# Kernel optimization log

Hardware: AMD Instinct MI355X
Metric: run time of the kernel (lower is better)

The kernel has to match this reference:

```python
import jax, jax.numpy as jnp
import numpy as np
from jax import lax

B, N, S, K = 16, 4096, 1024, 32
C_PTS = 64
MLP = [64, 64, 128]
BN_EPS = 1e-5


def _fps(xyz, npoint):
    """Farthest point sampling. xyz: [B,N,3] -> idx [B,npoint] int32."""
    b, n, _ = xyz.shape
    def body(carry, _):
        dist, farthest = carry                       # [B,N], [B]
        centroid = xyz[jnp.arange(b), farthest]      # [B,3]
        d = jnp.sum((xyz - centroid[:, None, :]) ** 2, axis=-1)  # [B,N]
        dist = jnp.minimum(dist, d)
        nxt = jnp.argmax(dist, axis=-1).astype(jnp.int32)
        return (dist, nxt), farthest
    init = (jnp.full((b, n), 1e10, dtype=xyz.dtype), jnp.zeros((b,), jnp.int32))
    _, idxs = lax.scan(body, init, None, length=npoint)  # [npoint, B]
    return idxs.T


def _gather(pts, idx):
    """pts: [B,N,C], idx: [B,S,K] -> [B,S,K,C] (per-batch gather)."""
    return jax.vmap(lambda p, i: p[i])(pts, idx)


def setup_inputs() -> dict:
    key = jax.random.key(0)
    ks = jax.random.split(key, 16)
    inp = {
        "xyz": jax.random.normal(ks[0], (B, N, 3), jnp.float32),
        "points": jax.random.normal(ks[1], (B, N, C_PTS), jnp.float32),
    }
    last = 3 + C_PTS
    ki = 2
    for i, out_c in enumerate(MLP):
        scale = 1.0 / np.sqrt(last)
        inp[f"w{i}"] = jax.random.normal(ks[ki], (last, out_c), jnp.float32) * scale
        inp[f"b{i}"] = jnp.zeros((out_c,), jnp.float32)
        inp[f"g{i}"] = jnp.ones((out_c,), jnp.float32)
        inp[f"be{i}"] = jnp.zeros((out_c,), jnp.float32)
        last = out_c
        ki += 1
    return inp


def _forward(xyz, points, params):
    fps_idx = _fps(xyz, S)                                    # [B,S]
    new_xyz = jnp.take_along_axis(xyz, fps_idx[..., None], axis=1)  # [B,S,3]
    # KNN: pairwise squared distances centroids -> all points
    d = (jnp.sum(new_xyz ** 2, -1)[:, :, None]
         - 2.0 * jnp.einsum('bsc,bnc->bsn', new_xyz, xyz)
         + jnp.sum(xyz ** 2, -1)[:, None, :])                 # [B,S,N]
    _, knn_idx = lax.top_k(-d, K)                             # [B,S,K]
    grouped_xyz = _gather(xyz, knn_idx) - new_xyz[:, :, None, :]   # [B,S,K,3]
    grouped_pts = _gather(points, knn_idx)                    # [B,S,K,C]
    x = jnp.concatenate([grouped_xyz, grouped_pts], axis=-1)  # [B,S,K,3+C]
    for (w, b, g, be) in params:
        x = jnp.einsum('bskc,cd->bskd', x, w) + b             # 1x1 conv
        mean = jnp.mean(x, axis=(0, 1, 2))                    # BN (train stats)
        var = jnp.var(x, axis=(0, 1, 2))
        x = (x - mean) * lax.rsqrt(var + BN_EPS) * g + be
        x = jax.nn.relu(x)
    new_points = jnp.max(x, axis=2)                           # max over nsample
    return new_xyz, new_points


def reference(xyz, points, w0, b0, g0, be0, w1, b1, g1, be1, w2, b2, g2, be2):
    params = [(w0, b0, g0, be0), (w1, b1, g1, be1), (w2, b2, g2, be2)]
    return _forward(xyz, points, params)
```

## Files before the change

### kernel.cpp

```cpp
#include <hip/hip_runtime.h>
#include <float.h>
#include <math.h>

#define B_ 16
#define N_ 4096
#define S_ 1024
#define K_ 32
#define CIN0 67
#define NBS (B_ * S_)
#define NEWXYZ_FLOATS (B_ * S_ * 3)
#define AST 68


__device__ __forceinline__ float sqdist3(float x, float y, float z,
                                         float cx, float cy, float cz) {
#pragma clang fp contract(off)
  float dx = x - cx, dy = y - cy, dz = z - cz;
  float s = dx * dx;
  s = s + dy * dy;
  s = s + dz * dz;
  return s;
}

__device__ __forceinline__ float knn_dist(float c2, float cx, float cy, float cz,
                                          float x, float y, float z) {
#pragma clang fp contract(off)
  float dot = cx * x; dot = dot + cy * y; dot = dot + cz * z;
  float x2 = x * x;   x2 = x2 + y * y;   x2 = x2 + z * z;
  float d = c2 - 2.0f * dot;
  d = d + x2;
  return d;
}

template <int CTRL>
__device__ __forceinline__ float dpp_f(float v, float oldv) {
  return __int_as_float(__builtin_amdgcn_update_dpp(
      __float_as_int(oldv), __float_as_int(v), CTRL, 0xF, 0xF, false));
}
template <int CTRL>
__device__ __forceinline__ int dpp_i(int v, int oldv) {
  return __builtin_amdgcn_update_dpp(oldv, v, CTRL, 0xF, 0xF, false);
}

template <int CTRL>
__device__ __forceinline__ void fps_combine2(float& val, int& idx) {
  const float tv = dpp_f<CTRL>(val, -1.0f);
  const int ti = dpp_i<CTRL>(idx, 0x7fffffff);
  const bool take = (tv > val) || (tv == val && ti < idx);
  val = take ? tv : val;
  idx = take ? ti : idx;
}

__global__ __launch_bounds__(256, 1) void fps_kernel(
    const float* __restrict__ xyz, float* __restrict__ newxyz) {
  const int b = blockIdx.x;
  const int t = threadIdx.x;
  __shared__ float4 sp[N_];
  __shared__ float2 rec[2][4];
  const float* xb = xyz + (size_t)b * N_ * 3;
  for (int p = t; p < N_; p += 256) {
    sp[p] = make_float4(xb[p * 3 + 0], xb[p * 3 + 1], xb[p * 3 + 2], 0.0f);
  }
  float ax[16], ay[16], az[16];
#pragma unroll
  for (int j = 0; j < 16; ++j) {
    const int p = t * 16 + j;
    const float x = xb[p * 3 + 0];
    const float y = xb[p * 3 + 1];
    const float z = xb[p * 3 + 2];
    asm volatile("v_accvgpr_write_b32 %0, %1" : "=a"(ax[j]) : "v"(x));
    asm volatile("v_accvgpr_write_b32 %0, %1" : "=a"(ay[j]) : "v"(y));
    asm volatile("v_accvgpr_write_b32 %0, %1" : "=a"(az[j]) : "v"(z));
  }
  float dist[16];
#pragma unroll
  for (int j = 0; j < 16; ++j) dist[j] = 1e10f;
  __syncthreads();
  float cx = xb[0], cy = xb[1], cz = xb[2];
  for (int s = 0; s < S_; ++s) {
    if (t == 0) {
      float* o = newxyz + ((size_t)b * S_ + s) * 3;
      o[0] = cx; o[1] = cy; o[2] = cz;
    }
    float dd[16];
#pragma unroll
    for (int j = 0; j < 16; ++j) {
      float x, y, z;
      asm volatile("v_accvgpr_read_b32 %0, %1" : "=v"(x) : "a"(ax[j]));
      asm volatile("v_accvgpr_read_b32 %0, %1" : "=v"(y) : "a"(ay[j]));
      asm volatile("v_accvgpr_read_b32 %0, %1" : "=v"(z) : "a"(az[j]));
      dd[j] = sqdist3(x, y, z, cx, cy, cz);
    }
    __builtin_amdgcn_sched_barrier(0);
    float best = -1.0f;
    int bi = 0;
#pragma unroll
    for (int j = 0; j < 16; ++j) {
      const float nd = fminf(dist[j], dd[j]);
      dist[j] = nd;
      const bool take = nd > best;
      best = take ? nd : best;
      bi = take ? (t * 16 + j) : bi;
    }
    fps_combine2<0x111>(best, bi);
    fps_combine2<0x112>(best, bi);
    fps_combine2<0x114>(best, bi);
    fps_combine2<0x118>(best, bi);
    fps_combine2<0x142>(best, bi);
    fps_combine2<0x143>(best, bi);
    const float wv = __int_as_float(__builtin_amdgcn_readlane(__float_as_int(best), 63));
    const int wi = __builtin_amdgcn_readlane(bi, 63);
    const int par = s & 1;
    if ((t & 63) == 0) {
      rec[par][t >> 6] = make_float2(wv, __int_as_float(wi));
    }
    __syncthreads();
    float2 r0 = rec[par][0];
    float bv = r0.x;
    int bj = __float_as_int(r0.y);
#pragma unroll
    for (int w = 1; w < 4; ++w) {
      const float2 r = rec[par][w];
      const int iw = __float_as_int(r.y);
      const bool take = (r.x > bv) || (r.x == bv && iw < bj);
      bv = take ? r.x : bv;
      bj = take ? iw : bj;
    }
    const float4 c = sp[bj];
    cx = c.x; cy = c.y; cz = c.z;
  }
}

__global__ __launch_bounds__(256, 2) void knn_kernel(
    const float* __restrict__ xyz, const float* __restrict__ newxyz,
    int* __restrict__ knn_idx) {
  const int bs0 = blockIdx.x * 4;
  const int b = bs0 >> 10;
  const int t = threadIdx.x;
  const int wave = t >> 6;
  const int lane = t & 63;
  __shared__ float sxx[N_];
  __shared__ float sxy[N_];
  __shared__ float sxz[N_];
  const float* xb = xyz + (size_t)b * N_ * 3;
  for (int p = t; p < N_; p += 256) {
    sxx[p] = xb[p * 3 + 0];
    sxy[p] = xb[p * 3 + 1];
    sxz[p] = xb[p * 3 + 2];
  }
  __syncthreads();
  const int bs = bs0 + wave;
  const float cx = newxyz[(size_t)bs * 3 + 0];
  const float cy = newxyz[(size_t)bs * 3 + 1];
  const float cz = newxyz[(size_t)bs * 3 + 2];
  float c2;
  {
#pragma clang fp contract(off)
    float s = cx * cx;
    s = s + cy * cy;
    s = s + cz * cz;
    c2 = s;
  }
  float d[64];
  float gval[8];
  int gidx[8];
#pragma unroll
  for (int g = 0; g < 8; ++g) {
    float gv = FLT_MAX;
    int gi = g * 8;
#pragma unroll
    for (int q = 0; q < 8; ++q) {
      const int j = g * 8 + q;
      const int p = j * 64 + lane;
      const float dd = knn_dist(c2, cx, cy, cz, sxx[p], sxy[p], sxz[p]);
      d[j] = dd;
      if (dd < gv) { gv = dd; gi = j; }
    }
    gval[g] = gv; gidx[g] = gi;
  }
  int* krow = knn_idx + (size_t)bs * K_;
  for (int it = 0; it < K_; ++it) {
    float best = gval[0];
    int bj = gidx[0];
#pragma unroll
    for (int g = 1; g < 8; ++g) {
      if (gval[g] < best || (gval[g] == best && gidx[g] < bj)) { best = gval[g]; bj = gidx[g]; }
    }
    int bidx = bj * 64 + lane;
#pragma unroll
    for (int off = 32; off >= 1; off >>= 1) {
      const float ov = __shfl_xor(best, off);
      const int oi = __shfl_xor(bidx, off);
      if (ov < best || (ov == best && oi < bidx)) { best = ov; bidx = oi; }
    }
    if (lane == 0) krow[it] = bidx;
    if (lane == (bidx & 63)) {
      const int jl = bidx >> 6;
      const int gg = jl >> 3;
      const int qq = jl & 7;
#pragma unroll
      for (int g = 0; g < 8; ++g) {
        if (g == gg) {
#pragma unroll
          for (int q = 0; q < 8; ++q) {
            d[g * 8 + q] = (q == qq) ? FLT_MAX : d[g * 8 + q];
          }
          float gv = FLT_MAX;
          int gi = g * 8;
#pragma unroll
          for (int q = 0; q < 8; ++q) {
            const int j = g * 8 + q;
            if (d[j] < gv) { gv = d[j]; gi = j; }
          }
          gval[g] = gv; gidx[g] = gi;
        }
      }
    }
  }
}


__device__ __forceinline__ void loadw(float* __restrict__ wbuf,
                                      const float* __restrict__ w, int n, int t) {
  for (int i = t; i < n; i += 256) wbuf[i] = w[i];
}

__device__ __forceinline__ void loadw_half(float* __restrict__ wbuf,
                                           const float* __restrict__ w2, int ofs, int t) {
  for (int i = t; i < 64 * 64; i += 256) {
    const int c = i >> 6, j = i & 63;
    wbuf[i] = w2[c * 128 + ofs + j];
  }
}

__device__ __forceinline__ void build_x0(float* __restrict__ act,
    const float* __restrict__ xyz, const float* __restrict__ points,
    const int* __restrict__ knn_idx, const float* __restrict__ newxyz,
    int bs, int t) {
  const int b = bs >> 10;
  const int* krow = knn_idx + (size_t)bs * K_;
  const float cx = newxyz[(size_t)bs * 3 + 0];
  const float cy = newxyz[(size_t)bs * 3 + 1];
  const float cz = newxyz[(size_t)bs * 3 + 2];
  for (int i = t; i < K_ * CIN0; i += 256) {
    const int k = i / CIN0;
    const int c = i - k * CIN0;
    const int p = krow[k];
    float v;
    if (c < 3) {
      v = xyz[((size_t)b * N_ + p) * 3 + c] - (c == 0 ? cx : (c == 1 ? cy : cz));
    } else {
      v = points[((size_t)b * N_ + p) * 64 + (c - 3)];
    }
    act[k * AST + c] = v;
  }
}

template <int CIN>
__device__ __forceinline__ void matmul64(const float* __restrict__ act,
    const float* __restrict__ wbuf, const float* __restrict__ bias,
    float* __restrict__ out, int t) {
  const int k = t >> 3;
  const int g = t & 7;
  float acc[8];
#pragma unroll
  for (int j = 0; j < 8; ++j) acc[j] = bias[g * 8 + j];
  for (int c = 0; c < CIN; ++c) {
    const float xv = act[k * AST + c];
#pragma unroll
    for (int j = 0; j < 8; ++j) acc[j] += xv * wbuf[c * 64 + g * 8 + j];
  }
#pragma unroll
  for (int j = 0; j < 8; ++j) out[k * AST + g * 8 + j] = acc[j];
}

__device__ __forceinline__ void norm_relu64(float* __restrict__ act,
    const float* __restrict__ scale, const float* __restrict__ shift, int t) {
  for (int i = t; i < K_ * 64; i += 256) {
    const int k = i >> 6, c = i & 63;
    const float v = act[k * AST + c] * scale[c] + shift[c];
    act[k * AST + c] = fmaxf(v, 0.0f);
  }
}

__device__ __forceinline__ void stats64(const float* __restrict__ out,
    float* __restrict__ psum, float* __restrict__ psq, int bs, int ofs, int t) {
  if (t < 64) {
    float s = 0.f, q = 0.f;
    for (int k = 0; k < K_; ++k) {
      const float v = out[k * AST + t];
      s += v; q += v * v;
    }
    psum[(size_t)bs * 128 + ofs + t] = s;
    psq[(size_t)bs * 128 + ofs + t] = q;
  }
}

__device__ __forceinline__ void minmax64(const float* __restrict__ out,
    float* __restrict__ maxraw, float* __restrict__ minbuf, int bs, int ofs, int t) {
  if (t >= 64 && t < 128) {
    const int ch = t - 64;
    float mx = -FLT_MAX, mn = FLT_MAX;
    for (int k = 0; k < K_; ++k) {
      const float v = out[k * AST + ch];
      mx = fmaxf(mx, v); mn = fminf(mn, v);
    }
    maxraw[(size_t)bs * 128 + ofs + ch] = mx;
    minbuf[(size_t)bs * 128 + ofs + ch] = mn;
  }
}


__global__ __launch_bounds__(256) void passA_store_kernel(
    const float* __restrict__ xyz, const float* __restrict__ points,
    const float* __restrict__ newxyz, const int* __restrict__ knn_idx,
    const float* __restrict__ w0, const float* __restrict__ b0,
    float* __restrict__ psum, float* __restrict__ psq, float* __restrict__ zbuf) {
  __shared__ float actA[K_ * AST];
  __shared__ float outB[K_ * AST];
  __shared__ float wbuf[CIN0 * 64];
  const int bs = blockIdx.x, t = threadIdx.x;
  build_x0(actA, xyz, points, knn_idx, newxyz, bs, t);
  loadw(wbuf, w0, CIN0 * 64, t);
  __syncthreads();
  matmul64<CIN0>(actA, wbuf, b0, outB, t);
  __syncthreads();
  stats64(outB, psum, psq, bs, 0, t);
  float* zrow = zbuf + (size_t)bs * 2048;
  for (int i = t; i < 2048; i += 256) zrow[i] = outB[(i >> 6) * AST + (i & 63)];
}

__global__ __launch_bounds__(256) void passB_z_kernel(
    const float* __restrict__ w1, const float* __restrict__ b1,
    const float* __restrict__ scales, const float* __restrict__ shifts,
    float* __restrict__ psum, float* __restrict__ psq, float* __restrict__ zbuf) {
  __shared__ float actA[K_ * AST];
  __shared__ float outB[K_ * AST];
  __shared__ float wbuf[64 * 64];
  const int bs = blockIdx.x, t = threadIdx.x;
  float* zrow = zbuf + (size_t)bs * 2048;
  for (int i = t; i < 2048; i += 256) outB[(i >> 6) * AST + (i & 63)] = zrow[i];
  loadw(wbuf, w1, 64 * 64, t);
  __syncthreads();
  norm_relu64(outB, scales, shifts, t);
  __syncthreads();
  matmul64<64>(outB, wbuf, b1, actA, t);
  __syncthreads();
  stats64(actA, psum, psq, bs, 0, t);
  for (int i = t; i < 2048; i += 256) zrow[i] = actA[(i >> 6) * AST + (i & 63)];
}

__global__ __launch_bounds__(256) void passC_z_kernel(
    const float* __restrict__ w2, const float* __restrict__ b2,
    const float* __restrict__ scales1, const float* __restrict__ shifts1,
    float* __restrict__ psum, float* __restrict__ psq,
    float* __restrict__ maxraw, float* __restrict__ minbuf,
    const float* __restrict__ zbuf) {
  __shared__ float actA[K_ * AST];
  __shared__ float outB[K_ * AST];
  __shared__ float wbuf[64 * 64];
  const int bs = blockIdx.x, t = threadIdx.x;
  const float* zrow = zbuf + (size_t)bs * 2048;
  for (int i = t; i < 2048; i += 256) actA[(i >> 6) * AST + (i & 63)] = zrow[i];
  loadw_half(wbuf, w2, 0, t);
  __syncthreads();
  norm_relu64(actA, scales1, shifts1, t);
  __syncthreads();
  matmul64<64>(actA, wbuf, b2, outB, t);
  __syncthreads();
  stats64(outB, psum, psq, bs, 0, t);
  minmax64(outB, maxraw, minbuf, bs, 0, t);
  loadw_half(wbuf, w2, 64, t);
  __syncthreads();
  matmul64<64>(actA, wbuf, b2 + 64, outB, t);
  __syncthreads();
  stats64(outB, psum, psq, bs, 64, t);
  minmax64(outB, maxraw, minbuf, bs, 64, t);
}


__global__ __launch_bounds__(256) void passA_kernel(
    const float* __restrict__ xyz, const float* __restrict__ points,
    const float* __restrict__ newxyz, const int* __restrict__ knn_idx,
    const float* __restrict__ w0, const float* __restrict__ b0,
    float* __restrict__ psum, float* __restrict__ psq) {
  __shared__ float actA[K_ * AST];
  __shared__ float outB[K_ * AST];
  __shared__ float wbuf[CIN0 * 64];
  const int bs = blockIdx.x, t = threadIdx.x;
  build_x0(actA, xyz, points, knn_idx, newxyz, bs, t);
  loadw(wbuf, w0, CIN0 * 64, t);
  __syncthreads();
  matmul64<CIN0>(actA, wbuf, b0, outB, t);
  __syncthreads();
  stats64(outB, psum, psq, bs, 0, t);
}

__global__ __launch_bounds__(256) void passB_kernel(
    const float* __restrict__ xyz, const float* __restrict__ points,
    const float* __restrict__ newxyz, const int* __restrict__ knn_idx,
    const float* __restrict__ w0, const float* __restrict__ b0,
    const float* __restrict__ w1, const float* __restrict__ b1,
    const float* __restrict__ scales, const float* __restrict__ shifts,
    float* __restrict__ psum, float* __restrict__ psq) {
  __shared__ float actA[K_ * AST];
  __shared__ float outB[K_ * AST];
  __shared__ float wbuf[CIN0 * 64];
  const int bs = blockIdx.x, t = threadIdx.x;
  build_x0(actA, xyz, points, knn_idx, newxyz, bs, t);
  loadw(wbuf, w0, CIN0 * 64, t);
  __syncthreads();
  matmul64<CIN0>(actA, wbuf, b0, outB, t);
  __syncthreads();
  norm_relu64(outB, scales, shifts, t);
  loadw(wbuf, w1, 64 * 64, t);
  __syncthreads();
  matmul64<64>(outB, wbuf, b1, actA, t);
  __syncthreads();
  stats64(actA, psum, psq, bs, 0, t);
}

__global__ __launch_bounds__(256) void passC_kernel(
    const float* __restrict__ xyz, const float* __restrict__ points,
    const float* __restrict__ newxyz, const int* __restrict__ knn_idx,
    const float* __restrict__ w0, const float* __restrict__ b0,
    const float* __restrict__ w1, const float* __restrict__ b1,
    const float* __restrict__ w2, const float* __restrict__ b2,
    const float* __restrict__ scales, const float* __restrict__ shifts,
    float* __restrict__ psum, float* __restrict__ psq,
    float* __restrict__ maxraw, float* __restrict__ minbuf) {
  __shared__ float actA[K_ * AST];
  __shared__ float outB[K_ * AST];
  __shared__ float wbuf[CIN0 * 64];
  const int bs = blockIdx.x, t = threadIdx.x;
  build_x0(actA, xyz, points, knn_idx, newxyz, bs, t);
  loadw(wbuf, w0, CIN0 * 64, t);
  __syncthreads();
  matmul64<CIN0>(actA, wbuf, b0, outB, t);
  __syncthreads();
  norm_relu64(outB, scales, shifts, t);
  loadw(wbuf, w1, 64 * 64, t);
  __syncthreads();
  matmul64<64>(outB, wbuf, b1, actA, t);
  __syncthreads();
  norm_relu64(actA, scales + 128, shifts + 128, t);
  loadw_half(wbuf, w2, 0, t);
  __syncthreads();
  matmul64<64>(actA, wbuf, b2, outB, t);
  __syncthreads();
  stats64(outB, psum, psq, bs, 0, t);
  minmax64(outB, maxraw, minbuf, bs, 0, t);
  loadw_half(wbuf, w2, 64, t);
  __syncthreads();
  matmul64<64>(actA, wbuf, b2 + 64, outB, t);
  __syncthreads();
  stats64(outB, psum, psq, bs, 64, t);
  minmax64(outB, maxraw, minbuf, bs, 64, t);
}

__global__ __launch_bounds__(256) void finalize_kernel(
    const float* __restrict__ psum, const float* __restrict__ psq,
    const float* __restrict__ g, const float* __restrict__ be,
    float* __restrict__ scale, float* __restrict__ shift) {
  const int ch = blockIdx.x, t = threadIdx.x;
  __shared__ float ss[256];
  __shared__ float sq[256];
  float s = 0.f, q = 0.f;
  for (int p = t; p < NBS; p += 256) {
    s += psum[(size_t)p * 128 + ch];
    q += psq[(size_t)p * 128 + ch];
  }
  ss[t] = s; sq[t] = q;
  __syncthreads();
  for (int off = 128; off >= 1; off >>= 1) {
    if (t < off) { ss[t] += ss[t + off]; sq[t] += sq[t + off]; }
    __syncthreads();
  }
  if (t == 0) {
    const float invN = 1.0f / (float)(B_ * S_ * K_);
    const float mean = ss[0] * invN;
    const float var = sq[0] * invN - mean * mean;
    const float sc = g[ch] / sqrtf(var + 1e-5f);
    scale[ch] = sc;
    shift[ch] = be[ch] - mean * sc;
  }
}

__global__ __launch_bounds__(256) void final_kernel(
    const float* __restrict__ minbuf, const float* __restrict__ scale,
    const float* __restrict__ shift, float* __restrict__ out) {
  const int i = blockIdx.x * 256 + threadIdx.x;
  const int ch = i & 127;
  const float sc = scale[ch], sh = shift[ch];
  const float mx = out[NEWXYZ_FLOATS + i];
  const float mn = minbuf[i];
  const float v = sc * (sc >= 0.f ? mx : mn) + sh;
  out[NEWXYZ_FLOATS + i] = fmaxf(v, 0.f);
}

extern "C" void kernel_launch(void* const* d_in, const int* in_sizes, int n_in,
                              void* d_out, int out_size, void* d_ws, size_t ws_size,
                              hipStream_t stream) {
  const float* xyz = (const float*)d_in[0];
  const float* points = (const float*)d_in[1];
  const float* w0 = (const float*)d_in[2];
  const float* b0 = (const float*)d_in[3];
  const float* g0 = (const float*)d_in[4];
  const float* be0 = (const float*)d_in[5];
  const float* w1 = (const float*)d_in[6];
  const float* b1 = (const float*)d_in[7];
  const float* g1 = (const float*)d_in[8];
  const float* be1 = (const float*)d_in[9];
  const float* w2 = (const float*)d_in[10];
  const float* b2 = (const float*)d_in[11];
  const float* g2 = (const float*)d_in[12];
  const float* be2 = (const float*)d_in[13];
  float* out = (float*)d_out;
  float* newxyz = out;
  float* maxraw = out + NEWXYZ_FLOATS;

  float* ws = (float*)d_ws;
  const size_t NEED_FAST =
      (size_t)(524288 + 16384 * 2048 + 2 * NBS * 128 + 768 + NBS * 128) * 4;

  fps_kernel<<<B_, 256, 0, stream>>>(xyz, newxyz);

  if (ws_size >= NEED_FAST) {
    int* knn_idx = (int*)ws;
    float* zbuf = ws + 524288;
    float* psum = zbuf + (size_t)16384 * 2048;
    float* psq = psum + (size_t)NBS * 128;
    float* scales = psq + (size_t)NBS * 128;
    float* shifts = scales + 384;
    float* minbuf = shifts + 384;
    knn_kernel<<<NBS / 4, 256, 0, stream>>>(xyz, newxyz, knn_idx);
    passA_store_kernel<<<NBS, 256, 0, stream>>>(xyz, points, newxyz, knn_idx, w0, b0,
                                                psum, psq, zbuf);
    finalize_kernel<<<64, 256, 0, stream>>>(psum, psq, g0, be0, scales, shifts);
    passB_z_kernel<<<NBS, 256, 0, stream>>>(w1, b1, scales, shifts, psum, psq, zbuf);
    finalize_kernel<<<64, 256, 0, stream>>>(psum, psq, g1, be1, scales + 128, shifts + 128);
    passC_z_kernel<<<NBS, 256, 0, stream>>>(w2, b2, scales + 128, shifts + 128,
                                            psum, psq, maxraw, minbuf, zbuf);
    finalize_kernel<<<128, 256, 0, stream>>>(psum, psq, g2, be2, scales + 256, shifts + 256);
    final_kernel<<<(B_ * S_ * 128) / 256, 256, 0, stream>>>(minbuf, scales + 256,
                                                            shifts + 256, out);
  } else {
    int* knn_idx = (int*)ws;
    float* psum = ws + 524288;
    float* psq = psum + (size_t)NBS * 128;
    float* scales = psq + (size_t)NBS * 128;
    float* shifts = scales + 384;
    float* minbuf = shifts + 384;
    knn_kernel<<<NBS / 4, 256, 0, stream>>>(xyz, newxyz, knn_idx);
    passA_kernel<<<NBS, 256, 0, stream>>>(xyz, points, newxyz, knn_idx, w0, b0, psum, psq);
    finalize_kernel<<<64, 256, 0, stream>>>(psum, psq, g0, be0, scales, shifts);
    passB_kernel<<<NBS, 256, 0, stream>>>(xyz, points, newxyz, knn_idx, w0, b0, w1, b1,
                                          scales, shifts, psum, psq);
    finalize_kernel<<<64, 256, 0, stream>>>(psum, psq, g1, be1, scales + 128, shifts + 128);
    passC_kernel<<<NBS, 256, 0, stream>>>(xyz, points, newxyz, knn_idx, w0, b0, w1, b1, w2, b2,
                                          scales, shifts, psum, psq, maxraw, minbuf);
    finalize_kernel<<<128, 256, 0, stream>>>(psum, psq, g2, be2, scales + 256, shifts + 256);
    final_kernel<<<(B_ * S_ * 128) / 256, 256, 0, stream>>>(minbuf, scales + 256,
                                                            shifts + 256, out);
  }
}
```

Measured before the change: 2.035 ms.

## Fuse FPS and KNN into persistent kernel with per-batch progress flags

Merges the serial FPS kernel and the KNN kernel into one persistent kernel. The first 16 blocks run FPS at raised priority and publish per-batch progress counters with release stores. The other blocks pull KNN tasks from an atomic queue and spin until the centroids they need exist, so KNN overlaps the long FPS phase instead of waiting for it to finish. The matmul inner loop also switches to float4 shared-memory loads with aligned buffers. The risks are spin-wait overhead, contention between the co-resident KNN blocks and the FPS blocks, and a dependence on all FPS blocks being resident, which could deadlock otherwise.

```diff
diff --git a/kernel.cpp b/kernel.cpp
--- a/kernel.cpp
+++ b/kernel.cpp
@@ -10,6 +10,7 @@
 #define NBS (B_ * S_)
 #define NEWXYZ_FLOATS (B_ * S_ * 3)
 #define AST 68
+#define TASKS 4096
 
 
 __device__ __forceinline__ float sqdist3(float x, float y, float z,
@@ -51,171 +52,194 @@
   idx = take ? ti : idx;
 }
 
-__global__ __launch_bounds__(256, 1) void fps_kernel(
-    const float* __restrict__ xyz, float* __restrict__ newxyz) {
-  const int b = blockIdx.x;
+__global__ __launch_bounds__(256, 2) void fused_fps_knn_kernel(
+    const float* __restrict__ xyz, float* __restrict__ newxyz,
+    int* __restrict__ knn_idx, int* __restrict__ ctrl) {
+  __shared__ float sx[N_];
+  __shared__ float sy[N_];
+  __shared__ float sz[N_];
+  __shared__ float2 rec[2][4];
+  __shared__ int sh_tq;
   const int t = threadIdx.x;
-  __shared__ float4 sp[N_];
-  __shared__ float2 rec[2][4];
-  const float* xb = xyz + (size_t)b * N_ * 3;
-  for (int p = t; p < N_; p += 256) {
-    sp[p] = make_float4(xb[p * 3 + 0], xb[p * 3 + 1], xb[p * 3 + 2], 0.0f);
-  }
-  float ax[16], ay[16], az[16];
-#pragma unroll
-  for (int j = 0; j < 16; ++j) {
-    const int p = t * 16 + j;
-    const float x = xb[p * 3 + 0];
-    const float y = xb[p * 3 + 1];
-    const float z = xb[p * 3 + 2];
-    asm volatile("v_accvgpr_write_b32 %0, %1" : "=a"(ax[j]) : "v"(x));
-    asm volatile("v_accvgpr_write_b32 %0, %1" : "=a"(ay[j]) : "v"(y));
-    asm volatile("v_accvgpr_write_b32 %0, %1" : "=a"(az[j]) : "v"(z));
-  }
-  float dist[16];
-#pragma unroll
-  for (int j = 0; j < 16; ++j) dist[j] = 1e10f;
-  __syncthreads();
-  float cx = xb[0], cy = xb[1], cz = xb[2];
-  for (int s = 0; s < S_; ++s) {
+
+  if (blockIdx.x < B_) {
+    __builtin_amdgcn_s_setprio(3);
+    const int b = blockIdx.x;
+    const float* xb = xyz + (size_t)b * N_ * 3;
+    for (int p = t; p < N_; p += 256) {
+      sx[p] = xb[p * 3 + 0];
+      sy[p] = xb[p * 3 + 1];
+      sz[p] = xb[p * 3 + 2];
+    }
+    float ax[16], ay[16], az[16];
+#pragma unroll
+    for (int j = 0; j < 16; ++j) {
+      const int p = t * 16 + j;
+      const float x = xb[p * 3 + 0];
+      const float y = xb[p * 3 + 1];
+      const float z = xb[p * 3 + 2];
+      asm volatile("v_accvgpr_write_b32 %0, %1" : "=a"(ax[j]) : "v"(x));
+      asm volatile("v_accvgpr_write_b32 %0, %1" : "=a"(ay[j]) : "v"(y));
+      asm volatile("v_accvgpr_write_b32 %0, %1" : "=a"(az[j]) : "v"(z));
+    }
+    float dist[16];
+#pragma unroll
+    for (int j = 0; j < 16; ++j) dist[j] = 1e10f;
+    __syncthreads();
+    float cx = xb[0], cy = xb[1], cz = xb[2];
+    for (int s = 0; s < S_; ++s) {
+      if (t == 0) {
+        float* o = newxyz + ((size_t)b * S_ + s) * 3;
+        o[0] = cx; o[1] = cy; o[2] = cz;
+        __hip_atomic_store(&ctrl[1 + b], s + 1, __ATOMIC_RELEASE,
+                           __HIP_MEMORY_SCOPE_AGENT);
+      }
+      float dd[16];
+#pragma unroll
+      for (int j = 0; j < 16; ++j) {
+        float x, y, z;
+        asm volatile("v_accvgpr_read_b32 %0, %1" : "=v"(x) : "a"(ax[j]));
+        asm volatile("v_accvgpr_read_b32 %0, %1" : "=v"(y) : "a"(ay[j]));
+        asm volatile("v_accvgpr_read_b32 %0, %1" : "=v"(z) : "a"(az[j]));
+        dd[j] = sqdist3(x, y, z, cx, cy, cz);
+      }
+      __builtin_amdgcn_sched_barrier(0);
+      float best = -1.0f;
+      int bi = 0;
+#pragma unroll
+      for (int j = 0; j < 16; ++j) {
+        const float nd = fminf(dist[j], dd[j]);
+        dist[j] = nd;
+        const bool take = nd > best;
+        best = take ? nd : best;
+        bi = take ? (t * 16 + j) : bi;
+      }
+      fps_combine2<0x111>(best, bi);
+      fps_combine2<0x112>(best, bi);
+      fps_combine2<0x114>(best, bi);
+      fps_combine2<0x118>(best, bi);
+      fps_combine2<0x142>(best, bi);
+      fps_combine2<0x143>(best, bi);
+      const float wv = __int_as_float(__builtin_amdgcn_readlane(__float_as_int(best), 63));
+      const int wi = __builtin_amdgcn_readlane(bi, 63);
+      const int par = s & 1;
+      if ((t & 63) == 0) {
+        rec[par][t >> 6] = make_float2(wv, __int_as_float(wi));
+      }
+      __syncthreads();
+      float2 r0 = rec[par][0];
+      float bv = r0.x;
+      int bj = __float_as_int(r0.y);
+#pragma unroll
+      for (int w = 1; w < 4; ++w) {
+        const float2 r = rec[par][w];
+        const int iw = __float_as_int(r.y);
+        const bool take = (r.x > bv) || (r.x == bv && iw < bj);
+        bv = take ? r.x : bv;
+        bj = take ? iw : bj;
+      }
+      cx = sx[bj]; cy = sy[bj]; cz = sz[bj];
+    }
+    __builtin_amdgcn_s_setprio(0);
+    __syncthreads();
+  }
+
+  while (true) {
+    if (t == 0) sh_tq = atomicAdd(&ctrl[0], 1);
+    __syncthreads();
+    const int tq = sh_tq;
+    if (tq >= TASKS) break;
+    const int b = tq & 15;
+    const int sg = tq >> 4;
     if (t == 0) {
-      float* o = newxyz + ((size_t)b * S_ + s) * 3;
-      o[0] = cx; o[1] = cy; o[2] = cz;
-    }
-    float dd[16];
-#pragma unroll
-    for (int j = 0; j < 16; ++j) {
-      float x, y, z;
-      asm volatile("v_accvgpr_read_b32 %0, %1" : "=v"(x) : "a"(ax[j]));
-      asm volatile("v_accvgpr_read_b32 %0, %1" : "=v"(y) : "a"(ay[j]));
-      asm volatile("v_accvgpr_read_b32 %0, %1" : "=v"(z) : "a"(az[j]));
-      dd[j] = sqdist3(x, y, z, cx, cy, cz);
-    }
-    __builtin_amdgcn_sched_barrier(0);
-    float best = -1.0f;
-    int bi = 0;
-#pragma unroll
-    for (int j = 0; j < 16; ++j) {
-      const float nd = fminf(dist[j], dd[j]);
-      dist[j] = nd;
-      const bool take = nd > best;
-      best = take ? nd : best;
-      bi = take ? (t * 16 + j) : bi;
-    }
-    fps_combine2<0x111>(best, bi);
-    fps_combine2<0x112>(best, bi);
-    fps_combine2<0x114>(best, bi);
-    fps_combine2<0x118>(best, bi);
-    fps_combine2<0x142>(best, bi);
-    fps_combine2<0x143>(best, bi);
-    const float wv = __int_as_float(__builtin_amdgcn_readlane(__float_as_int(best), 63));
-    const int wi = __builtin_amdgcn_readlane(bi, 63);
-    const int par = s & 1;
-    if ((t & 63) == 0) {
-      rec[par][t >> 6] = make_float2(wv, __int_as_float(wi));
-    }
-    __syncthreads();
-    float2 r0 = rec[par][0];
-    float bv = r0.x;
-    int bj = __float_as_int(r0.y);
-#pragma unroll
-    for (int w = 1; w < 4; ++w) {
-      const float2 r = rec[par][w];
-      const int iw = __float_as_int(r.y);
-      const bool take = (r.x > bv) || (r.x == bv && iw < bj);
-      bv = take ? r.x : bv;
-      bj = take ? iw : bj;
-    }
-    const float4 c = sp[bj];
-    cx = c.x; cy = c.y; cz = c.z;
-  }
-}
-
-__global__ __launch_bounds__(256, 2) void knn_kernel(
-    const float* __restrict__ xyz, const float* __restrict__ newxyz,
-    int* __restrict__ knn_idx) {
-  const int bs0 = blockIdx.x * 4;
-  const int b = bs0 >> 10;
-  const int t = threadIdx.x;
-  const int wave = t >> 6;
-  const int lane = t & 63;
-  __shared__ float sxx[N_];
-  __shared__ float sxy[N_];
-  __shared__ float sxz[N_];
-  const float* xb = xyz + (size_t)b * N_ * 3;
-  for (int p = t; p < N_; p += 256) {
-    sxx[p] = xb[p * 3 + 0];
-    sxy[p] = xb[p * 3 + 1];
-    sxz[p] = xb[p * 3 + 2];
-  }
-  __syncthreads();
-  const int bs = bs0 + wave;
-  const float cx = newxyz[(size_t)bs * 3 + 0];
-  const float cy = newxyz[(size_t)bs * 3 + 1];
-  const float cz = newxyz[(size_t)bs * 3 + 2];
-  float c2;
-  {
+      while (__hip_atomic_load(&ctrl[1 + b], __ATOMIC_ACQUIRE,
+                               __HIP_MEMORY_SCOPE_AGENT) < sg * 4 + 4) {
+        __builtin_amdgcn_s_sleep(2);
+      }
+    }
+    __syncthreads();
+    const float* xb = xyz + (size_t)b * N_ * 3;
+    for (int p = t; p < N_; p += 256) {
+      sx[p] = xb[p * 3 + 0];
+      sy[p] = xb[p * 3 + 1];
+      sz[p] = xb[p * 3 + 2];
+    }
+    __syncthreads();
+    {
+      const int wave = t >> 6;
+      const int lane = t & 63;
+      const int bs = b * S_ + sg * 4 + wave;
+      const float cx = newxyz[(size_t)bs * 3 + 0];
+      const float cy = newxyz[(size_t)bs * 3 + 1];
+      const float cz = newxyz[(size_t)bs * 3 + 2];
+      float c2;
+      {
 #pragma clang fp contract(off)
-    float s = cx * cx;
-    s = s + cy * cy;
-    s = s + cz * cz;
-    c2 = s;
-  }
-  float d[64];
-  float gval[8];
-  int gidx[8];
-#pragma unroll
-  for (int g = 0; g < 8; ++g) {
-    float gv = FLT_MAX;
-    int gi = g * 8;
-#pragma unroll
-    for (int q = 0; q < 8; ++q) {
-      const int j = g * 8 + q;
-      const int p = j * 64 + lane;
-      const float dd = knn_dist(c2, cx, cy, cz, sxx[p], sxy[p], sxz[p]);
-      d[j] = dd;
-      if (dd < gv) { gv = dd; gi = j; }
-    }
-    gval[g] = gv; gidx[g] = gi;
-  }
-  int* krow = knn_idx + (size_t)bs * K_;
-  for (int it = 0; it < K_; ++it) {
-    float best = gval[0];
-    int bj = gidx[0];
-#pragma unroll
-    for (int g = 1; g < 8; ++g) {
-      if (gval[g] < best || (gval[g] == best && gidx[g] < bj)) { best = gval[g]; bj = gidx[g]; }
-    }
-    int bidx = bj * 64 + lane;
-#pragma unroll
-    for (int off = 32; off >= 1; off >>= 1) {
-      const float ov = __shfl_xor(best, off);
-      const int oi = __shfl_xor(bidx, off);
-      if (ov < best || (ov == best && oi < bidx)) { best = ov; bidx = oi; }
-    }
-    if (lane == 0) krow[it] = bidx;
-    if (lane == (bidx & 63)) {
-      const int jl = bidx >> 6;
-      const int gg = jl >> 3;
-      const int qq = jl & 7;
+        float s = cx * cx;
+        s = s + cy * cy;
+        s = s + cz * cz;
+        c2 = s;
+      }
+      float d[64];
+      float gval[8];
+      int gidx[8];
 #pragma unroll
       for (int g = 0; g < 8; ++g) {
-        if (g == gg) {
-#pragma unroll
-          for (int q = 0; q < 8; ++q) {
-            d[g * 8 + q] = (q == qq) ? FLT_MAX : d[g * 8 + q];
+        float gv = FLT_MAX;
+        int gi = g * 8;
+#pragma unroll
+        for (int q = 0; q < 8; ++q) {
+          const int j = g * 8 + q;
+          const int p = j * 64 + lane;
+          const float dd = knn_dist(c2, cx, cy, cz, sx[p], sy[p], sz[p]);
+          d[j] = dd;
+          if (dd < gv) { gv = dd; gi = j; }
+        }
+        gval[g] = gv; gidx[g] = gi;
+      }
+      int* krow = knn_idx + (size_t)bs * K_;
+      for (int it = 0; it < K_; ++it) {
+        float best = gval[0];
+        int bj = gidx[0];
+#pragma unroll
+        for (int g = 1; g < 8; ++g) {
+          if (gval[g] < best || (gval[g] == best && gidx[g] < bj)) {
+            best = gval[g]; bj = gidx[g];
           }
-          float gv = FLT_MAX;
-          int gi = g * 8;
-#pragma unroll
-          for (int q = 0; q < 8; ++q) {
-            const int j = g * 8 + q;
-            if (d[j] < gv) { gv = d[j]; gi = j; }
+        }
+        int bidx = bj * 64 + lane;
+#pragma unroll
+        for (int off = 32; off >= 1; off >>= 1) {
+          const float ov = __shfl_xor(best, off);
+          const int oi = __shfl_xor(bidx, off);
+          if (ov < best || (ov == best && oi < bidx)) { best = ov; bidx = oi; }
+        }
+        if (lane == 0) krow[it] = bidx;
+        if (lane == (bidx & 63)) {
+          const int jl = bidx >> 6;
+          const int gg = jl >> 3;
+          const int qr = jl & 7;
+#pragma unroll
+          for (int g = 0; g < 8; ++g) {
+            if (g == gg) {
+#pragma unroll
+              for (int q = 0; q < 8; ++q) {
+                d[g * 8 + q] = (q == qr) ? FLT_MAX : d[g * 8 + q];
+              }
+              float gv = FLT_MAX;
+              int gi = g * 8;
+#pragma unroll
+              for (int q = 0; q < 8; ++q) {
+                const int j = g * 8 + q;
+                if (d[j] < gv) { gv = d[j]; gi = j; }
+              }
+              gval[g] = gv; gidx[g] = gi;
+            }
           }
-          gval[g] = gv; gidx[g] = gi;
         }
       }
     }
+    __syncthreads();
   }
 }
 
@@ -267,11 +291,15 @@
   for (int j = 0; j < 8; ++j) acc[j] = bias[g * 8 + j];
   for (int c = 0; c < CIN; ++c) {
     const float xv = act[k * AST + c];
-#pragma unroll
-    for (int j = 0; j < 8; ++j) acc[j] += xv * wbuf[c * 64 + g * 8 + j];
-  }
-#pragma unroll
-  for (int j = 0; j < 8; ++j) out[k * AST + g * 8 + j] = acc[j];
+    const float4 wa = *(const float4*)&wbuf[c * 64 + g * 8];
+    const float4 wb = *(const float4*)&wbuf[c * 64 + g * 8 + 4];
+    acc[0] += xv * wa.x; acc[1] += xv * wa.y;
+    acc[2] += xv * wa.z; acc[3] += xv * wa.w;
+    acc[4] += xv * wb.x; acc[5] += xv * wb.y;
+    acc[6] += xv * wb.z; acc[7] += xv * wb.w;
+  }
+  *(float4*)&out[k * AST + g * 8] = make_float4(acc[0], acc[1], acc[2], acc[3]);
+  *(float4*)&out[k * AST + g * 8 + 4] = make_float4(acc[4], acc[5], acc[6], acc[7]);
 }
 
 __device__ __forceinline__ void norm_relu64(float* __restrict__ act,
@@ -316,9 +344,9 @@
     const float* __restrict__ newxyz, const int* __restrict__ knn_idx,
     const float* __restrict__ w0, const float* __restrict__ b0,
     float* __restrict__ psum, float* __restrict__ psq, float* __restrict__ zbuf) {
-  __shared__ float actA[K_ * AST];
-  __shared__ float outB[K_ * AST];
-  __shared__ float wbuf[CIN0 * 64];
+  __shared__ __align__(16) float actA[K_ * AST];
+  __shared__ __align__(16) float outB[K_ * AST];
+  __shared__ __align__(16) float wbuf[CIN0 * 64];
   const int bs = blockIdx.x, t = threadIdx.x;
   build_x0(actA, xyz, points, knn_idx, newxyz, bs, t);
   loadw(wbuf, w0, CIN0 * 64, t);
@@ -334,9 +362,9 @@
     const float* __restrict__ w1, const float* __restrict__ b1,
     const float* __restrict__ scales, const float* __restrict__ shifts,
     float* __restrict__ psum, float* __restrict__ psq, float* __restrict__ zbuf) {
-  __shared__ float actA[K_ * AST];
-  __shared__ float outB[K_ * AST];
-  __shared__ float wbuf[64 * 64];
+  __shared__ __align__(16) float actA[K_ * AST];
+  __shared__ __align__(16) float outB[K_ * AST];
+  __shared__ __align__(16) float wbuf[64 * 64];
   const int bs = blockIdx.x, t = threadIdx.x;
   float* zrow = zbuf + (size_t)bs * 2048;
   for (int i = t; i < 2048; i += 256) outB[(i >> 6) * AST + (i & 63)] = zrow[i];
@@ -356,9 +384,9 @@
     float* __restrict__ psum, float* __restrict__ psq,
     float* __restrict__ maxraw, float* __restrict__ minbuf,
     const float* __restrict__ zbuf) {
-  __shared__ float actA[K_ * AST];
-  __shared__ float outB[K_ * AST];
-  __shared__ float wbuf[64 * 64];
+  __shared__ __align__(16) float actA[K_ * AST];
+  __shared__ __align__(16) float outB[K_ * AST];
+  __shared__ __align__(16) float wbuf[64 * 64];
   const int bs = blockIdx.x, t = threadIdx.x;
   const float* zrow = zbuf + (size_t)bs * 2048;
   for (int i = t; i < 2048; i += 256) actA[(i >> 6) * AST + (i & 63)] = zrow[i];
@@ -384,9 +412,9 @@
     const float* __restrict__ newxyz, const int* __restrict__ knn_idx,
     const float* __restrict__ w0, const float* __restrict__ b0,
     float* __restrict__ psum, float* __restrict__ psq) {
-  __shared__ float actA[K_ * AST];
-  __shared__ float outB[K_ * AST];
-  __shared__ float wbuf[CIN0 * 64];
+  __shared__ __align__(16) float actA[K_ * AST];
+  __shared__ __align__(16) float outB[K_ * AST];
+  __shared__ __align__(16) float wbuf[CIN0 * 64];
   const int bs = blockIdx.x, t = threadIdx.x;
   build_x0(actA, xyz, points, knn_idx, newxyz, bs, t);
   loadw(wbuf, w0, CIN0 * 64, t);
@@ -403,9 +431,9 @@
     const float* __restrict__ w1, const float* __restrict__ b1,
     const float* __restrict__ scales, const float* __restrict__ shifts,
     float* __restrict__ psum, float* __restrict__ psq) {
-  __shared__ float actA[K_ * AST];
-  __shared__ float outB[K_ * AST];
-  __shared__ float wbuf[CIN0 * 64];
+  __shared__ __align__(16) float actA[K_ * AST];
+  __shared__ __align__(16) float outB[K_ * AST];
+  __shared__ __align__(16) float wbuf[CIN0 * 64];
   const int bs = blockIdx.x, t = threadIdx.x;
   build_x0(actA, xyz, points, knn_idx, newxyz, bs, t);
   loadw(wbuf, w0, CIN0 * 64, t);
@@ -429,9 +457,9 @@
     const float* __restrict__ scales, const float* __restrict__ shifts,
     float* __restrict__ psum, float* __restrict__ psq,
     float* __restrict__ maxraw, float* __restrict__ minbuf) {
-  __shared__ float actA[K_ * AST];
-  __shared__ float outB[K_ * AST];
-  __shared__ float wbuf[CIN0 * 64];
+  __shared__ __align__(16) float actA[K_ * AST];
+  __shared__ __align__(16) float outB[K_ * AST];
+  __shared__ __align__(16) float wbuf[CIN0 * 64];
   const int bs = blockIdx.x, t = threadIdx.x;
   build_x0(actA, xyz, points, knn_idx, newxyz, bs, t);
   loadw(wbuf, w0, CIN0 * 64, t);
@@ -520,20 +548,21 @@
   float* maxraw = out + NEWXYZ_FLOATS;
 
   float* ws = (float*)d_ws;
+  int* ctrl = (int*)ws;
+  int* knn_idx = (int*)ws + 64;
   const size_t NEED_FAST =
-      (size_t)(524288 + 16384 * 2048 + 2 * NBS * 128 + 768 + NBS * 128) * 4;
-
-  fps_kernel<<<B_, 256, 0, stream>>>(xyz, newxyz);
+      (size_t)(64 + 524288 + 16384 * 2048 + 2 * NBS * 128 + 768 + NBS * 128) * 4;
+
+  hipMemsetAsync(ctrl, 0, 256, stream);
+  fused_fps_knn_kernel<<<512, 256, 0, stream>>>(xyz, newxyz, knn_idx, ctrl);
 
   if (ws_size >= NEED_FAST) {
-    int* knn_idx = (int*)ws;
-    float* zbuf = ws + 524288;
+    float* zbuf = ws + 64 + 524288;
     float* psum = zbuf + (size_t)16384 * 2048;
     float* psq = psum + (size_t)NBS * 128;
     float* scales = psq + (size_t)NBS * 128;
     float* shifts = scales + 384;
     float* minbuf = shifts + 384;
-    knn_kernel<<<NBS / 4, 256, 0, stream>>>(xyz, newxyz, knn_idx);
     passA_store_kernel<<<NBS, 256, 0, stream>>>(xyz, points, newxyz, knn_idx, w0, b0,
                                                 psum, psq, zbuf);
     finalize_kernel<<<64, 256, 0, stream>>>(psum, psq, g0, be0, scales, shifts);
@@ -545,13 +574,11 @@
     final_kernel<<<(B_ * S_ * 128) / 256, 256, 0, stream>>>(minbuf, scales + 256,
                                                             shifts + 256, out);
   } else {
-    int* knn_idx = (int*)ws;
-    float* psum = ws + 524288;
+    float* psum = ws + 64 + 524288;
     float* psq = psum + (size_t)NBS * 128;
     float* scales = psq + (size_t)NBS * 128;
     float* shifts = scales + 384;
     float* minbuf = shifts + 384;
-    knn_kernel<<<NBS / 4, 256, 0, stream>>>(xyz, newxyz, knn_idx);
     passA_kernel<<<NBS, 256, 0, stream>>>(xyz, points, newxyz, knn_idx, w0, b0, psum, psq);
     finalize_kernel<<<64, 256, 0, stream>>>(psum, psq, g0, be0, scales, shifts);
     passB_kernel<<<NBS, 256, 0, stream>>>(xyz, points, newxyz, knn_idx, w0, b0, w1, b1,
```

New measurement: 5.463 ms. +168.5%, slower.
